# Kernel tuning notes

Hardware: AMD Instinct MI355X
Metric: run time of the kernel (lower is better)

## Reference

```python
import jax, jax.numpy as jnp
import numpy as np


def setup_inputs() -> dict:
    key = jax.random.key(0)
    k1, k2 = jax.random.split(key)
    d, T, n = 256, 8192, 64
    # scale down so exp(ht^T D^T D hj) stays in range, as typical trained D would
    H = jax.random.normal(k1, (d, T), dtype=jnp.float32) * 0.1
    D = jax.random.normal(k2, (n, d), dtype=jnp.float32) * 0.1
    l2 = jnp.ones((), dtype=jnp.float32)
    return {"H": H, "D": D, "l2": l2}


def reference(H, D, l2):
    # H: [d, T], D: [n, d]
    DH = D @ H                                   # [n, T] = D @ H_T.T
    # S[t, j] = h_t^T (D^T D) h_j  == (DH)^T (DH)
    S = jnp.einsum('nt,nj->tj', DH, DH)          # [T, T]
    # beta_j = exp(-0.5 * ||D h_j||^2); row t: attn[t,:] = beta * exp(S[t,:]) / sum
    log_beta = -0.5 * jnp.sum(DH * DH, axis=0)   # [T]
    attn_map = jax.nn.softmax(S + log_beta[None, :], axis=1)  # [T, T]
    Z = l2 * (H @ attn_map)                      # [d, T]
    return Z
```

## Files before the change

kernel.cpp:

```cpp
#include <hip/hip_runtime.h>

#define T_DIM 8192
#define D_DIM 256
#define N_DIM 64
#define LOG2E 1.44269504f

typedef __bf16 bf16x8 __attribute__((ext_vector_type(8)));
typedef __bf16 bf16x4 __attribute__((ext_vector_type(4)));
typedef float f32x16 __attribute__((ext_vector_type(16)));

__device__ __forceinline__ f32x16 zero16() {
  f32x16 v;
#pragma unroll
  for (int i = 0; i < 16; ++i) v[i] = 0.f;
  return v;
}


__global__ __launch_bounds__(256) void k_dh(const float* __restrict__ H,
                                            const float* __restrict__ Dm,
                                            __bf16* __restrict__ DHf,
                                            float* __restrict__ lbe,
                                            float* __restrict__ rowsum) {
  __shared__ __bf16 HlThi[64 * 264];
  __shared__ __bf16 HlTlo[64 * 264];
  __shared__ __bf16 DHs[64 * 72];
  const int tid = threadIdx.x;
  const int t0 = blockIdx.x * 64;
  const int lane = tid & 63;
  const int wave = tid >> 6;
  const int h = lane >> 5;
  const int l31 = lane & 31;
  const float4* H4 = (const float4*)H;
#pragma unroll
  for (int r = 0; r < 16; ++r) {
    int idx = r * 256 + tid;
    int d = idx >> 4, tc = idx & 15;
    float4 v = H4[(size_t)d * (T_DIM / 4) + (t0 >> 2) + tc];
    float vv[4] = {v.x, v.y, v.z, v.w};
#pragma unroll
    for (int i = 0; i < 4; ++i) {
      __bf16 hi = (__bf16)vv[i];
      float lo = vv[i] - (float)hi;
      HlThi[(tc * 4 + i) * 264 + d] = hi;
      HlTlo[(tc * 4 + i) * 264 + d] = (__bf16)lo;
    }
  }
  __syncthreads();
  const int tt = wave & 1, nh = wave >> 1;
  const int m = tt * 32 + l31;
  const int n = nh * 32 + l31;
  f32x16 c = zero16();
  for (int kk = 0; kk < 16; ++kk) {
    bf16x8 ahi = *(const bf16x8*)&HlThi[m * 264 + kk * 16 + h * 8];
    bf16x8 alo = *(const bf16x8*)&HlTlo[m * 264 + kk * 16 + h * 8];
    const float4* dp = (const float4*)(Dm + (size_t)n * 256 + kk * 16 + h * 8);
    float4 b0 = dp[0], b1 = dp[1];
    float bv[8] = {b0.x, b0.y, b0.z, b0.w, b1.x, b1.y, b1.z, b1.w};
    bf16x8 bhi, blo;
#pragma unroll
    for (int i = 0; i < 8; ++i) {
      __bf16 hi = (__bf16)bv[i];
      bhi[i] = hi;
      blo[i] = (__bf16)(bv[i] - (float)hi);
    }
    c = __builtin_amdgcn_mfma_f32_32x32x16_bf16(ahi, bhi, c, 0, 0, 0);
    c = __builtin_amdgcn_mfma_f32_32x32x16_bf16(ahi, blo, c, 0, 0, 0);
    c = __builtin_amdgcn_mfma_f32_32x32x16_bf16(alo, bhi, c, 0, 0, 0);
  }
#pragma unroll
  for (int r = 0; r < 16; ++r) {
    int row = tt * 32 + (r & 3) + 8 * (r >> 2) + 4 * h;
    DHs[row * 72 + n] = (__bf16)c[r];
  }
  __syncthreads();
#pragma unroll
  for (int r = 0; r < 2; ++r) {
    int idx = r * 256 + tid;
    int g = idx >> 8, cc = (idx >> 5) & 7, l = idx & 31;
    bf16x8 w = *(const bf16x8*)&DHs[(g * 32 + l) * 72 + cc * 8];
    *(bf16x8*)(DHf + (size_t)(blockIdx.x * 2 + g) * 2048 + cc * 256 + l * 8) = w;
  }
  if (tid < 64) {
    float s = 0.f;
#pragma unroll
    for (int q = 0; q < 8; ++q) {
      bf16x8 w = *(const bf16x8*)&DHs[tid * 72 + q * 8];
#pragma unroll
      for (int i = 0; i < 8; ++i) { float f = (float)w[i]; s += f * f; }
    }
    lbe[t0 + tid] = -0.5f * s * LOG2E;
    rowsum[t0 + tid] = 0.f;
  }
}

__global__ __launch_bounds__(512, 4) void k_rowsum(const __bf16* __restrict__ DHf,
                                                   const float* __restrict__ lbe,
                                                   float* __restrict__ rowsum) {
  __shared__ float red2[256][33];
  const int tid = threadIdx.x;
  const int lane = tid & 63;
  const int wave = tid >> 6;
  const int h = lane >> 5;
  const int l31 = lane & 31;
  const int t0 = (int)(blockIdx.x >> 4) * 256;
  const int jbase = (int)(blockIdx.x & 15) * 512;
  const size_t Gt = (size_t)(t0 >> 5) + wave;
  bf16x8 aR[4];
#pragma unroll
  for (int kk = 0; kk < 4; ++kk)
    aR[kk] = *(const bf16x8*)(DHf + Gt * 2048 + kk * 512 + lane * 8);
  float racc[16];
#pragma unroll
  for (int r = 0; r < 16; ++r) racc[r] = 0.f;
  bf16x8 b[4];
  {
    const size_t Gj = (size_t)(jbase >> 5);
#pragma unroll
    for (int kk = 0; kk < 4; ++kk)
      b[kk] = *(const bf16x8*)(DHf + Gj * 2048 + kk * 512 + lane * 8);
  }
  for (int jit = 0; jit < 16; ++jit) {
    bf16x8 bn[4];
    if (jit < 15) {
      const size_t Gj = (size_t)(jbase >> 5) + jit + 1;
#pragma unroll
      for (int kk = 0; kk < 4; ++kk)
        bn[kk] = *(const bf16x8*)(DHf + Gj * 2048 + kk * 512 + lane * 8);
    }
    const float lbv = lbe[jbase + jit * 32 + l31];
    f32x16 s = zero16();
    s = __builtin_amdgcn_mfma_f32_32x32x16_bf16(aR[0], b[0], s, 0, 0, 0);
    s = __builtin_amdgcn_mfma_f32_32x32x16_bf16(aR[1], b[1], s, 0, 0, 0);
    s = __builtin_amdgcn_mfma_f32_32x32x16_bf16(aR[2], b[2], s, 0, 0, 0);
    s = __builtin_amdgcn_mfma_f32_32x32x16_bf16(aR[3], b[3], s, 0, 0, 0);
#pragma unroll
    for (int r = 0; r < 16; ++r)
      racc[r] += __builtin_amdgcn_exp2f(__builtin_fmaf(s[r], LOG2E, lbv));
    if (jit < 15) {
#pragma unroll
      for (int kk = 0; kk < 4; ++kk) b[kk] = bn[kk];
    }
  }
#pragma unroll
  for (int r = 0; r < 16; ++r) {
    int tl = wave * 32 + (r & 3) + 8 * (r >> 2) + 4 * h;
    red2[tl][l31] = racc[r];
  }
  __syncthreads();
  if (tid < 256) {
    float s = 0.f;
#pragma unroll 8
    for (int c = 0; c < 32; ++c) s += red2[tid][c];
    atomicAdd(&rowsum[t0 + tid], s);
  }
}

__global__ __launch_bounds__(256) void k_scaleH(const float* __restrict__ H,
                                                const float* __restrict__ rowsum,
                                                __bf16* __restrict__ Hbf_sw,
                                                float* __restrict__ Z) {
  __shared__ float rinvL[64];
  const int tid = threadIdx.x;
  const int bx = blockIdx.x;
  const int tblk = bx >> 1, dh = bx & 1;
  const int t0 = tblk * 64;
  if (tid < 64) rinvL[tid] = 1.0f / rowsum[t0 + tid];
  __syncthreads();
#pragma unroll
  for (int itr = 0; itr < 4; ++itr) {
    int idx = itr * 256 + tid;
    int dl = idx >> 3, tbp = idx & 7;
    int d = dh * 128 + dl;
    int swz = (d ^ (d >> 3)) & 7;
    int tloc = (tbp ^ swz) << 3;
    const float4* hp = (const float4*)(H + (size_t)d * T_DIM + t0 + tloc);
    float4 v0 = hp[0], v1 = hp[1];
    float4 r0 = *(const float4*)&rinvL[tloc];
    float4 r1 = *(const float4*)&rinvL[tloc + 4];
    bf16x8 w;
    w[0] = (__bf16)(v0.x * r0.x); w[1] = (__bf16)(v0.y * r0.y);
    w[2] = (__bf16)(v0.z * r0.z); w[3] = (__bf16)(v0.w * r0.w);
    w[4] = (__bf16)(v1.x * r1.x); w[5] = (__bf16)(v1.y * r1.y);
    w[6] = (__bf16)(v1.z * r1.z); w[7] = (__bf16)(v1.w * r1.w);
    *(bf16x8*)(Hbf_sw + (size_t)tblk * 16384 + (size_t)d * 64 + tbp * 8) = w;
  }
  float4* Z4 = (float4*)Z;
  const int base = bx * 256 + tid;
  const float4 z4 = {0.f, 0.f, 0.f, 0.f};
#pragma unroll
  for (int r = 0; r < 8; ++r) Z4[r * 65536 + base] = z4;
}

__global__ __launch_bounds__(256, 2) void k_z(const __bf16* __restrict__ Hbf_sw,
                                              const __bf16* __restrict__ DHf,
                                              const float* __restrict__ lbe,
                                              const float* __restrict__ l2p,
                                              float* __restrict__ Z) {
  __shared__ __bf16 Hs[2][128 * 64];
  __shared__ __bf16 Pt[2][128 * 64];
  const int tid = threadIdx.x;
  const int lane = tid & 63;
  const int wave = tid >> 6;
  const int h = lane >> 5;
  const int l31 = lane & 31;
  const int bx = blockIdx.x;
  const int ts = bx & 3;
  const int dh = (bx >> 2) & 1;
  const int j0 = (bx >> 3) * 128;
  const float l2v = l2p[0];
  const int s_tt = wave & 1, s_jg = wave >> 1;
  bf16x8 bS[2][4];
  float lbv[2];
#pragma unroll
  for (int q = 0; q < 2; ++q) {
    const size_t Gj = (j0 >> 5) + s_jg * 2 + q;
#pragma unroll
    for (int kk = 0; kk < 4; ++kk)
      bS[q][kk] = *(const bf16x8*)(DHf + Gj * 2048 + kk * 512 + lane * 8);
    lbv[q] = lbe[j0 + (s_jg * 2 + q) * 32 + l31];
  }
  f32x16 acc[2][2];
#pragma unroll
  for (int u = 0; u < 2; ++u)
#pragma unroll
    for (int v = 0; v < 2; ++v) acc[u][v] = zero16();

#define DMA_HS(buf_, it_)                                                       \
  {                                                                             \
    const __bf16* gsrc =                                                        \
        Hbf_sw + (size_t)(ts * 32 + (it_)) * 16384 + (size_t)dh * 8192;         \
    _Pragma("unroll") for (int r = 0; r < 4; ++r) {                             \
      int chunk = wave * 4 + r;                                                 \
      __builtin_amdgcn_global_load_lds(                                         \
          (const __attribute__((address_space(1))) unsigned int*)(gsrc +        \
              chunk * 512 + lane * 8),                                          \
          (__attribute__((address_space(3))) unsigned int*)(&Hs[buf_][0] +      \
              chunk * 512),                                                     \
          16, 0, 0);                                                            \
    }                                                                           \
  }

#define S_PHASE(p_)                                                             \
  {                                                                             \
    _Pragma("unroll") for (int q = 0; q < 2; ++q) {                             \
      f32x16 s = zero16();                                                      \
      _Pragma("unroll") for (int kk = 0; kk < 4; ++kk)                          \
          s = __builtin_amdgcn_mfma_f32_32x32x16_bf16(aR[kk], bS[q][kk], s, 0,  \
                                                      0, 0);                    \
      const int jl = (s_jg * 2 + q) * 32 + l31;                                 \
      const int sj = (jl ^ (jl >> 3)) & 7;                                      \
      _Pragma("unroll") for (int g = 0; g < 4; ++g) {                           \
        const int tl = s_tt * 32 + g * 8 + 4 * h;                               \
        bf16x4 pv;                                                              \
        pv[0] = (__bf16)__builtin_amdgcn_exp2f(                                 \
            __builtin_fmaf(s[g * 4 + 0], LOG2E, lbv[q]));                       \
        pv[1] = (__bf16)__builtin_amdgcn_exp2f(                                 \
            __builtin_fmaf(s[g * 4 + 1], LOG2E, lbv[q]));                       \
        pv[2] = (__bf16)__builtin_amdgcn_exp2f(                                 \
            __builtin_fmaf(s[g * 4 + 2], LOG2E, lbv[q]));                       \
        pv[3] = (__bf16)__builtin_amdgcn_exp2f(                                 \
            __builtin_fmaf(s[g * 4 + 3], LOG2E, lbv[q]));                       \
        const int cchunk = tl >> 3;                                             \
        *(bf16x4*)&Pt[p_][jl * 64 + ((cchunk ^ sj) << 3) + 4 * h] = pv;         \
      }                                                                         \
    }                                                                           \
  }

  bf16x8 aR[4];
#pragma unroll
  for (int kk = 0; kk < 4; ++kk)
    aR[kk] = *(const bf16x8*)(DHf + (size_t)(ts * 64 + s_tt) * 2048 + kk * 512 + lane * 8);
  DMA_HS(0, 0);
  S_PHASE(0);
#pragma unroll
  for (int kk = 0; kk < 4; ++kk)
    aR[kk] = *(const bf16x8*)(DHf + (size_t)(ts * 64 + 2 + s_tt) * 2048 + kk * 512 + lane * 8);
  __syncthreads();

  for (int it = 0; it < 32; ++it) {
    const int p = it & 1;
    if (it < 31) {
      DMA_HS(p ^ 1, it + 1);
      S_PHASE(p ^ 1);
    }
    if (it < 30) {
      const size_t Gt = ts * 64 + (it + 2) * 2 + s_tt;
#pragma unroll
      for (int kk = 0; kk < 4; ++kk)
        aR[kk] = *(const bf16x8*)(DHf + Gt * 2048 + kk * 512 + lane * 8);
    }
#pragma unroll
    for (int kk = 0; kk < 4; ++kk) {
      const int c = kk * 2 + h;
      bf16x8 af[2], bw[2];
#pragma unroll
      for (int u = 0; u < 2; ++u) {
        int dl = (wave & 1) * 64 + u * 32 + l31;
        af[u] = *(const bf16x8*)&Hs[p][dl * 64 + ((c ^ ((dl ^ (dl >> 3)) & 7)) << 3)];
      }
#pragma unroll
      for (int v = 0; v < 2; ++v) {
        int j = (wave >> 1) * 64 + v * 32 + l31;
        bw[v] = *(const bf16x8*)&Pt[p][j * 64 + ((c ^ ((j ^ (j >> 3)) & 7)) << 3)];
      }
#pragma unroll
      for (int u = 0; u < 2; ++u)
#pragma unroll
        for (int v = 0; v < 2; ++v)
          acc[u][v] = __builtin_amdgcn_mfma_f32_32x32x16_bf16(af[u], bw[v], acc[u][v], 0, 0, 0);
    }
    __syncthreads();
  }
#undef S_PHASE
#undef DMA_HS
#pragma unroll
  for (int u = 0; u < 2; ++u)
#pragma unroll
    for (int v = 0; v < 2; ++v)
#pragma unroll
      for (int r = 0; r < 16; ++r) {
        int d = dh * 128 + (wave & 1) * 64 + u * 32 + (r & 3) + 8 * (r >> 2) + 4 * h;
        int j = j0 + (wave >> 1) * 64 + v * 32 + l31;
        atomicAdd(&Z[(size_t)d * T_DIM + j], acc[u][v][r] * l2v);
      }
}

extern "C" void kernel_launch(void* const* d_in, const int* in_sizes, int n_in,
                              void* d_out, int out_size, void* d_ws,
                              size_t ws_size, hipStream_t stream) {
  (void)in_sizes; (void)n_in; (void)out_size; (void)ws_size;
  const float* H = (const float*)d_in[0];
  const float* Dm = (const float*)d_in[1];
  const float* l2 = (const float*)d_in[2];
  float* Z = (float*)d_out;
  char* ws = (char*)d_ws;
  __bf16* DHf = (__bf16*)ws;
  float* lbe = (float*)(ws + 1048576);
  float* rowsum = (float*)(ws + 1048576 + 32768);
  __bf16* Hbf_sw = (__bf16*)(ws + 1048576 + 65536);

  k_dh<<<128, 256, 0, stream>>>(H, Dm, DHf, lbe, rowsum);
  k_rowsum<<<512, 512, 0, stream>>>(DHf, lbe, rowsum);
  k_scaleH<<<256, 256, 0, stream>>>(H, rowsum, Hbf_sw, Z);
  k_z<<<512, 256, 0, stream>>>(Hbf_sw, DHf, lbe, l2, Z);
}
```

Before: 159.7 us.

## Replace Z atomics with split-T partial buffers plus reduction kernel, unroll main loop

The Z accumulation across the four T-splits no longer uses float atomicAdd into a zeroed output. Each split now writes its own partial Z buffer, and a new reduction kernel sums the four partials and applies l2, so the Z zeroing in k_scaleH is removed. The k_z main loop is unrolled by two with double-buffered aR registers, and the MFMA phase is wrapped in s_setprio. This trades atomic traffic for an extra 32MB partial write/read and one more kernel launch.

Measured after the change: 145.7 us. -8.8%, faster.

```diff
diff --git a/kernel.cpp b/kernel.cpp
--- a/kernel.cpp
+++ b/kernel.cpp
@@ -158,8 +158,7 @@
 
 __global__ __launch_bounds__(256) void k_scaleH(const float* __restrict__ H,
                                                 const float* __restrict__ rowsum,
-                                                __bf16* __restrict__ Hbf_sw,
-                                                float* __restrict__ Z) {
+                                                __bf16* __restrict__ Hbf_sw) {
   __shared__ float rinvL[64];
   const int tid = threadIdx.x;
   const int bx = blockIdx.x;
@@ -185,18 +184,12 @@
     w[6] = (__bf16)(v1.z * r1.z); w[7] = (__bf16)(v1.w * r1.w);
     *(bf16x8*)(Hbf_sw + (size_t)tblk * 16384 + (size_t)d * 64 + tbp * 8) = w;
   }
-  float4* Z4 = (float4*)Z;
-  const int base = bx * 256 + tid;
-  const float4 z4 = {0.f, 0.f, 0.f, 0.f};
-#pragma unroll
-  for (int r = 0; r < 8; ++r) Z4[r * 65536 + base] = z4;
 }
 
 __global__ __launch_bounds__(256, 2) void k_z(const __bf16* __restrict__ Hbf_sw,
                                               const __bf16* __restrict__ DHf,
                                               const float* __restrict__ lbe,
-                                              const float* __restrict__ l2p,
-                                              float* __restrict__ Z) {
+                                              float* __restrict__ Zp) {
   __shared__ __bf16 Hs[2][128 * 64];
   __shared__ __bf16 Pt[2][128 * 64];
   const int tid = threadIdx.x;
@@ -208,7 +201,6 @@
   const int ts = bx & 3;
   const int dh = (bx >> 2) & 1;
   const int j0 = (bx >> 3) * 128;
-  const float l2v = l2p[0];
   const int s_tt = wave & 1, s_jg = wave >> 1;
   bf16x8 bS[2][4];
   float lbv[2];
@@ -241,13 +233,20 @@
     }                                                                           \
   }
 
-#define S_PHASE(p_)                                                             \
+#define LOAD_AR(reg_, n_)                                                       \
+  {                                                                             \
+    const size_t Gt_ = (size_t)(ts * 64 + (n_)*2 + s_tt);                       \
+    _Pragma("unroll") for (int kk = 0; kk < 4; ++kk)                            \
+        (reg_)[kk] = *(const bf16x8*)(DHf + Gt_ * 2048 + kk * 512 + lane * 8);  \
+  }
+
+#define S_PHASE(p_, reg_)                                                       \
   {                                                                             \
     _Pragma("unroll") for (int q = 0; q < 2; ++q) {                             \
       f32x16 s = zero16();                                                      \
       _Pragma("unroll") for (int kk = 0; kk < 4; ++kk)                          \
-          s = __builtin_amdgcn_mfma_f32_32x32x16_bf16(aR[kk], bS[q][kk], s, 0,  \
-                                                      0, 0);                    \
+          s = __builtin_amdgcn_mfma_f32_32x32x16_bf16((reg_)[kk], bS[q][kk], s, \
+                                                      0, 0, 0);                 \
       const int jl = (s_jg * 2 + q) * 32 + l31;                                 \
       const int sj = (jl ^ (jl >> 3)) & 7;                                      \
       _Pragma("unroll") for (int g = 0; g < 4; ++g) {                           \
@@ -267,53 +266,57 @@
     }                                                                           \
   }
 
-  bf16x8 aR[4];
-#pragma unroll
-  for (int kk = 0; kk < 4; ++kk)
-    aR[kk] = *(const bf16x8*)(DHf + (size_t)(ts * 64 + s_tt) * 2048 + kk * 512 + lane * 8);
+#define Z_PHASE(p_)                                                             \
+  {                                                                             \
+    __builtin_amdgcn_s_setprio(1);                                              \
+    _Pragma("unroll") for (int kk = 0; kk < 4; ++kk) {                          \
+      const int c = kk * 2 + h;                                                 \
+      bf16x8 af[2], bw[2];                                                      \
+      _Pragma("unroll") for (int u = 0; u < 2; ++u) {                           \
+        int dl = (wave & 1) * 64 + u * 32 + l31;                                \
+        af[u] =                                                                 \
+            *(const bf16x8*)&Hs[p_][dl * 64 + ((c ^ ((dl ^ (dl >> 3)) & 7)) << 3)]; \
+      }                                                                         \
+      _Pragma("unroll") for (int v = 0; v < 2; ++v) {                           \
+        int j = (wave >> 1) * 64 + v * 32 + l31;                                \
+        bw[v] =                                                                 \
+            *(const bf16x8*)&Pt[p_][j * 64 + ((c ^ ((j ^ (j >> 3)) & 7)) << 3)]; \
+      }                                                                         \
+      _Pragma("unroll") for (int u = 0; u < 2; ++u)                             \
+          _Pragma("unroll") for (int v = 0; v < 2; ++v)                         \
+              acc[u][v] = __builtin_amdgcn_mfma_f32_32x32x16_bf16(              \
+                  af[u], bw[v], acc[u][v], 0, 0, 0);                            \
+    }                                                                           \
+    __builtin_amdgcn_s_setprio(0);                                              \
+  }
+
+  bf16x8 aR[4], aRn[4];
+  LOAD_AR(aR, 0);
   DMA_HS(0, 0);
-  S_PHASE(0);
-#pragma unroll
-  for (int kk = 0; kk < 4; ++kk)
-    aR[kk] = *(const bf16x8*)(DHf + (size_t)(ts * 64 + 2 + s_tt) * 2048 + kk * 512 + lane * 8);
-  __syncthreads();
-
-  for (int it = 0; it < 32; ++it) {
-    const int p = it & 1;
-    if (it < 31) {
-      DMA_HS(p ^ 1, it + 1);
-      S_PHASE(p ^ 1);
-    }
-    if (it < 30) {
-      const size_t Gt = ts * 64 + (it + 2) * 2 + s_tt;
-#pragma unroll
-      for (int kk = 0; kk < 4; ++kk)
-        aR[kk] = *(const bf16x8*)(DHf + Gt * 2048 + kk * 512 + lane * 8);
-    }
-#pragma unroll
-    for (int kk = 0; kk < 4; ++kk) {
-      const int c = kk * 2 + h;
-      bf16x8 af[2], bw[2];
-#pragma unroll
-      for (int u = 0; u < 2; ++u) {
-        int dl = (wave & 1) * 64 + u * 32 + l31;
-        af[u] = *(const bf16x8*)&Hs[p][dl * 64 + ((c ^ ((dl ^ (dl >> 3)) & 7)) << 3)];
-      }
-#pragma unroll
-      for (int v = 0; v < 2; ++v) {
-        int j = (wave >> 1) * 64 + v * 32 + l31;
-        bw[v] = *(const bf16x8*)&Pt[p][j * 64 + ((c ^ ((j ^ (j >> 3)) & 7)) << 3)];
-      }
-#pragma unroll
-      for (int u = 0; u < 2; ++u)
-#pragma unroll
-        for (int v = 0; v < 2; ++v)
-          acc[u][v] = __builtin_amdgcn_mfma_f32_32x32x16_bf16(af[u], bw[v], acc[u][v], 0, 0, 0);
-    }
+  S_PHASE(0, aR);
+  LOAD_AR(aRn, 1);
+  __syncthreads();
+
+  for (int ii = 0; ii < 16; ++ii) {
+    const int it0 = ii * 2;
+    DMA_HS(1, it0 + 1);
+    if (it0 < 30) LOAD_AR(aR, it0 + 2);
+    S_PHASE(1, aRn);
+    Z_PHASE(0);
     __syncthreads();
-  }
+    if (it0 + 1 < 31) {
+      DMA_HS(0, it0 + 2);
+      S_PHASE(0, aR);
+    }
+    if (it0 + 1 < 30) LOAD_AR(aRn, it0 + 3);
+    Z_PHASE(1);
+    __syncthreads();
+  }
+#undef Z_PHASE
 #undef S_PHASE
+#undef LOAD_AR
 #undef DMA_HS
+  float* zp = Zp + (size_t)ts * (256 * (size_t)T_DIM);
 #pragma unroll
   for (int u = 0; u < 2; ++u)
 #pragma unroll
@@ -322,8 +325,24 @@
       for (int r = 0; r < 16; ++r) {
         int d = dh * 128 + (wave & 1) * 64 + u * 32 + (r & 3) + 8 * (r >> 2) + 4 * h;
         int j = j0 + (wave >> 1) * 64 + v * 32 + l31;
-        atomicAdd(&Z[(size_t)d * T_DIM + j], acc[u][v][r] * l2v);
+        zp[(size_t)d * T_DIM + j] = acc[u][v][r];
       }
+}
+
+__global__ __launch_bounds__(256) void k_zred(const float* __restrict__ Zp,
+                                              const float* __restrict__ l2p,
+                                              float* __restrict__ Z) {
+  const int i = blockIdx.x * 256 + threadIdx.x;
+  const float l2v = l2p[0];
+  const float4* zp4 = (const float4*)Zp;
+  float4 a = zp4[i];
+#pragma unroll
+  for (int s = 1; s < 4; ++s) {
+    float4 b = zp4[(size_t)s * 524288 + i];
+    a.x += b.x; a.y += b.y; a.z += b.z; a.w += b.w;
+  }
+  float4 o = {a.x * l2v, a.y * l2v, a.z * l2v, a.w * l2v};
+  ((float4*)Z)[i] = o;
 }
 
 extern "C" void kernel_launch(void* const* d_in, const int* in_sizes, int n_in,
@@ -338,10 +357,12 @@
   __bf16* DHf = (__bf16*)ws;
   float* lbe = (float*)(ws + 1048576);
   float* rowsum = (float*)(ws + 1048576 + 32768);
-  __bf16* Hbf_sw = (__bf16*)(ws + 1048576 + 65536);
+  __bf16* Hbf_sw = (__bf16*)(ws + 1114112);
+  float* Zp = (float*)(ws + 5308416);
 
   k_dh<<<128, 256, 0, stream>>>(H, Dm, DHf, lbe, rowsum);
   k_rowsum<<<512, 512, 0, stream>>>(DHf, lbe, rowsum);
-  k_scaleH<<<256, 256, 0, stream>>>(H, rowsum, Hbf_sw, Z);
-  k_z<<<512, 256, 0, stream>>>(Hbf_sw, DHf, lbe, l2, Z);
-}
+  k_scaleH<<<256, 256, 0, stream>>>(H, rowsum, Hbf_sw);
+  k_z<<<512, 256, 0, stream>>>(Hbf_sw, DHf, lbe, Zp);
+  k_zred<<<2048, 256, 0, stream>>>(Zp, l2, Z);
+}
```
